# Kernel optimization log

Hardware: AMD Instinct MI355X
Metric: run time of the kernel (lower is better)

## Reference

```python
import jax, jax.numpy as jnp
import numpy as np

N = 20000
E = 500000
NS = 128
NT = 128
BN_EPS = 1e-3
DIMS = [NS, 2 * NT, 4 * NT, 2 * NT, NT, NT]


def setup_inputs() -> dict:
    key = jax.random.key(0)
    ks = jax.random.split(key, 32)
    inp = {
        "x": jax.random.normal(ks[0], (N, NS), jnp.float32),
        "edge_index": jax.random.randint(ks[1], (2, E), 0, N),
        "edge_attr": jax.random.uniform(ks[2], (E,), jnp.float32),
    }
    for i in range(5):
        din, dout = DIMS[i], DIMS[i + 1]
        inp[f"W{i+1}"] = jax.random.normal(ks[3 + i], (din, dout), jnp.float32) * (1.0 / np.sqrt(din)).astype(np.float32)
        inp[f"b{i+1}"] = jnp.zeros((dout,), jnp.float32)
    for i in range(4):
        d = DIMS[i + 1]
        inp[f"g{i+1}"] = 1.0 + 0.1 * jax.random.normal(ks[10 + i], (d,), jnp.float32)
        inp[f"be{i+1}"] = 0.1 * jax.random.normal(ks[14 + i], (d,), jnp.float32)
        inp[f"m{i+1}"] = 0.1 * jax.random.normal(ks[18 + i], (d,), jnp.float32)
        inp[f"v{i+1}"] = jax.random.uniform(ks[22 + i], (d,), jnp.float32, minval=0.5, maxval=1.5)
    return inp


def gcn_norm(edge_index, edge_attr, n):
    # PyG gcn_norm with self-loops (fill value 1) and symmetric degree norm.
    loop = jnp.arange(n)
    row = jnp.concatenate([edge_index[0], loop])
    col = jnp.concatenate([edge_index[1], loop])
    w = jnp.concatenate([edge_attr, jnp.ones((n,), edge_attr.dtype)])
    deg = jax.ops.segment_sum(w, col, num_segments=n)
    dinv = jnp.where(deg > 0, jax.lax.rsqrt(deg), 0.0)
    return row, col, dinv[row] * w * dinv[col]


def gcn_conv(h, W, b, row, col, norm, n):
    # out[col] += norm * (h @ W)[row]; then add bias (PyG GCNConv).
    hw = h @ W
    agg = jax.ops.segment_sum(hw[row] * norm[:, None], col, num_segments=n)
    return agg + b


def bn_eval(h, g, be, m, v):
    return (h - m) * jax.lax.rsqrt(v + BN_EPS) * g + be


def reference(x, edge_index, edge_attr,
              W1, b1, W2, b2, W3, b3, W4, b4, W5, b5,
              g1, be1, m1, v1, g2, be2, m2, v2,
              g3, be3, m3, v3, g4, be4, m4, v4):
    n = x.shape[0]
    row, col, norm = gcn_norm(edge_index, edge_attr, n)  # cached=True: shared by all layers
    h = jax.nn.sigmoid(bn_eval(gcn_conv(x, W1, b1, row, col, norm, n), g1, be1, m1, v1))
    h = jax.nn.sigmoid(bn_eval(gcn_conv(h, W2, b2, row, col, norm, n), g2, be2, m2, v2))
    h = jax.nn.sigmoid(bn_eval(gcn_conv(h, W3, b3, row, col, norm, n), g3, be3, m3, v3))
    h = jax.nn.sigmoid(bn_eval(gcn_conv(h, W4, b4, row, col, norm, n), g4, be4, m4, v4))
    h = jax.nn.sigmoid(gcn_conv(h, W5, b5, row, col, norm, n))
    # dropout is identity in eval mode
    x11 = h.T @ h  # [NT, NT]
    x12 = 0.5 * (x11 + x11.T)
    return x12 - jnp.diag(jnp.diag(x12))
```

## Files before the change

### kernel.cpp

```cpp
#include <hip/hip_runtime.h>
#include <hip/hip_bf16.h>
#include <hip/hip_fp8.h>
#include <cstdint>
#include <cstddef>

typedef __hip_bfloat16 bf16;
typedef unsigned char fp8;
typedef __attribute__((ext_vector_type(8))) short short8;
typedef __attribute__((ext_vector_type(4))) float f32x4;
typedef __attribute__((ext_vector_type(2))) float f32x2;

#define NSF 128
#define BN_EPS 1e-3f
#define NR 4
#define SCK 2048


__global__ void passA_kernel(const int* __restrict__ ei, int* __restrict__ fill,
                             int* __restrict__ loc, int E, int n, int rsize) {
    int idx = blockIdx.x * blockDim.x + threadIdx.x;
    if (idx < E) {
        int r = ei[idx];
        int c = ei[E + idx];
        int slot = c * NR + r / rsize;
        loc[idx] = atomicAdd(&fill[slot], 1);
    } else if (idx < E + n) {
        int i = idx - E;
        int slot = i * NR + i / rsize;
        loc[idx] = atomicAdd(&fill[slot], 1);
    }
}


__global__ void scan1_kernel(const int* __restrict__ cnt, int* __restrict__ blksum, int total) {
    __shared__ int red[256];
    int base = blockIdx.x * SCK + threadIdx.x * 8;
    int s = 0;
    #pragma unroll
    for (int i = 0; i < 8; ++i) {
        int idx = base + i;
        if (idx < total) s += cnt[idx];
    }
    red[threadIdx.x] = s;
    __syncthreads();
    for (int off2 = 128; off2 > 0; off2 >>= 1) {
        if (threadIdx.x < off2) red[threadIdx.x] += red[threadIdx.x + off2];
        __syncthreads();
    }
    if (threadIdx.x == 0) blksum[blockIdx.x] = red[0];
}

__global__ void scan2_kernel(int* __restrict__ blksum, int* __restrict__ row_ptr,
                             int nblk, int total) {
    __shared__ int part[256];
    int tid = threadIdx.x;
    int v = (tid < nblk) ? blksum[tid] : 0;
    part[tid] = v;
    __syncthreads();
    for (int off2 = 1; off2 < 256; off2 <<= 1) {
        int t = (tid >= off2) ? part[tid - off2] : 0;
        __syncthreads();
        part[tid] += t;
        __syncthreads();
    }
    if (tid < nblk) blksum[tid] = part[tid] - v;
    if (tid == 255) row_ptr[total] = part[255];
}

__global__ void scan3_kernel(const int* __restrict__ cnt, const int* __restrict__ blkoff,
                             int* __restrict__ row_ptr, int total) {
    __shared__ int part[256];
    int tid = threadIdx.x;
    int base = blockIdx.x * SCK + tid * 8;
    int loc[8]; int s = 0;
    #pragma unroll
    for (int i = 0; i < 8; ++i) {
        int idx = base + i;
        loc[i] = (idx < total) ? cnt[idx] : 0;
        s += loc[i];
    }
    part[tid] = s;
    __syncthreads();
    for (int off2 = 1; off2 < 256; off2 <<= 1) {
        int t = (tid >= off2) ? part[tid - off2] : 0;
        __syncthreads();
        part[tid] += t;
        __syncthreads();
    }
    int run = blkoff[blockIdx.x] + part[tid] - s;
    #pragma unroll
    for (int i = 0; i < 8; ++i) {
        int idx = base + i;
        if (idx < total) { row_ptr[idx] = run; run += loc[i]; }
    }
}

__global__ void passB_kernel(const int* __restrict__ ei, const float* __restrict__ ea,
                             const int* __restrict__ row_ptr, const int* __restrict__ loc,
                             int2* __restrict__ e8, int* __restrict__ csr_col,
                             int E, int n, int rsize) {
    int idx = blockIdx.x * blockDim.x + threadIdx.x;
    if (idx < E) {
        int r = ei[idx];
        int c = ei[E + idx];
        int slot = c * NR + r / rsize;
        int p = row_ptr[slot] + loc[idx];
        int2 rec; rec.x = r; rec.y = __float_as_int(ea[idx]);
        e8[p] = rec;
        csr_col[p] = c;
    } else if (idx < E + n) {
        int i = idx - E;
        int slot = i * NR + i / rsize;
        int p = row_ptr[slot] + loc[idx];
        int2 rec; rec.x = i; rec.y = __float_as_int(1.0f);
        e8[p] = rec;
        csr_col[p] = i;
    }
}

__global__ void degdinv_kernel(const int* __restrict__ row_ptr, const int2* __restrict__ e8,
                               float* __restrict__ dinv, int n) {
    int node = blockIdx.x * blockDim.x + threadIdx.x;
    if (node < n) {
        int s = row_ptr[node * NR], e = row_ptr[(node + 1) * NR];
        float d = 0.0f;
        for (int j = s; j < e; ++j) d += __int_as_float(e8[j].y);
        dinv[node] = (d > 0.0f) ? rsqrtf(d) : 0.0f;
    }
}

__global__ void normw_kernel(const float* __restrict__ dinv, const int* __restrict__ csr_col,
                             int2* __restrict__ e8, int EN) {
    int p = blockIdx.x * blockDim.x + threadIdx.x;
    if (p < EN) {
        int2 rec = e8[p];
        float w = dinv[rec.x] * __int_as_float(rec.y) * dinv[csr_col[p]];
        ((int*)e8)[2 * p + 1] = __float_as_int(w);
    }
}


__device__ inline void store_val(bf16* C, size_t idx, float a) {
    C[idx] = __float2bfloat16(a);
}
__device__ inline void store_val(fp8* C, size_t idx, float a) {
    int packed = __builtin_amdgcn_cvt_pk_fp8_f32(a, a, 0, false);
    C[idx] = (fp8)(packed & 0xff);
}

__global__ void prep_kernel(int* __restrict__ fill, int total,
                            const float* __restrict__ x, fp8* __restrict__ xq, int xcnt,
                            const float* __restrict__ W0, const float* __restrict__ W1,
                            const float* __restrict__ W2, const float* __restrict__ W3,
                            const float* __restrict__ W4,
                            bf16* __restrict__ wtbuf, int wtelems) {
    int idx = blockIdx.x * blockDim.x + threadIdx.x;
    if (idx < total) { fill[idx] = 0; return; }
    idx -= total;
    if (idx < xcnt) {
        store_val(xq, idx, x[idx]);
        return;
    }
    int widx = idx - xcnt;
    if (widx >= wtelems) return;
    const float* W; int K, off;
    if (widx < 32768)       { W = W0; K = 128; off = 0; }
    else if (widx < 163840) { W = W1; K = 256; off = 32768; }
    else if (widx < 294912) { W = W2; K = 512; off = 163840; }
    else if (widx < 327680) { W = W3; K = 256; off = 294912; }
    else                    { W = W4; K = 128; off = 327680; }
    int N2;
    if (widx < 32768) N2 = 256; else if (widx < 163840) N2 = 512;
    else if (widx < 294912) N2 = 256; else N2 = 128;
    int l = widx - off;
    int nn = l / K, kk = l % K;
    wtbuf[widx] = __float2bfloat16(W[(size_t)kk * N2 + nn]);
}


__device__ inline void gl_lds16(const bf16* g, bf16* l) {
    __builtin_amdgcn_global_load_lds(
        (const __attribute__((address_space(1))) void*)g,
        (__attribute__((address_space(3))) void*)l,
        16, 0, 0);
}


template <typename OT>
__global__ __launch_bounds__(256) void mfma_gemm_kernel(
    const bf16* __restrict__ A, const bf16* __restrict__ Wt,
    OT* __restrict__ C, int M, int K, int N, int mode,
    const float* __restrict__ bias, const float* __restrict__ g,
    const float* __restrict__ be, const float* __restrict__ m,
    const float* __restrict__ v) {
    __shared__ bf16 As[64][32];
    __shared__ bf16 Bs[128][32];
    int m0 = blockIdx.x * 64;
    int n0 = blockIdx.y * 128;
    int tid = threadIdx.x;
    int wave = tid >> 6, lane = tid & 63;
    int lrow = lane & 15, quad = lane >> 4;

    f32x4 acc[4][2] = {};

    int srow = lane >> 2;
    int sseg = lane & 3;
    int am = wave * 16 + srow;
    int bn = wave * 32 + srow;
    bool aok = (m0 + am) < M;

    for (int k0 = 0; k0 < K; k0 += 32) {
        if (aok)
            gl_lds16(A + (size_t)(m0 + am) * K + k0 + sseg * 8, &As[am][sseg * 8]);
        gl_lds16(Wt + (size_t)(n0 + bn) * K + k0 + sseg * 8, &Bs[bn][sseg * 8]);
        gl_lds16(Wt + (size_t)(n0 + bn + 16) * K + k0 + sseg * 8, &Bs[bn + 16][sseg * 8]);
        __syncthreads();

        short8 afrag[4], bfrag[2];
        #pragma unroll
        for (int mt = 0; mt < 4; ++mt)
            afrag[mt] = *(const short8*)(&As[mt * 16 + lrow][quad * 8]);
        #pragma unroll
        for (int nt = 0; nt < 2; ++nt)
            bfrag[nt] = *(const short8*)(&Bs[wave * 32 + nt * 16 + lrow][quad * 8]);
        #pragma unroll
        for (int mt = 0; mt < 4; ++mt)
            #pragma unroll
            for (int nt = 0; nt < 2; ++nt)
                acc[mt][nt] = __builtin_amdgcn_mfma_f32_16x16x32_bf16(
                    afrag[mt], bfrag[nt], acc[mt][nt], 0, 0, 0);
        __syncthreads();
    }
    #pragma unroll
    for (int nt = 0; nt < 2; ++nt) {
        int gn = n0 + wave * 32 + nt * 16 + lrow;
        float bsc = 0.0f, scale = 1.0f, mean = 0.0f, beta = 0.0f;
        if (mode == 1) {
            bsc = bias[gn];
            scale = g[gn] * rsqrtf(v[gn] + BN_EPS);
            mean = m[gn];
            beta = be[gn];
        }
        #pragma unroll
        for (int mt = 0; mt < 4; ++mt) {
            #pragma unroll
            for (int rr = 0; rr < 4; ++rr) {
                int gm = m0 + mt * 16 + quad * 4 + rr;
                if (gm < M) {
                    float a = acc[mt][nt][rr];
                    if (mode == 1) {
                        a = (a + bsc - mean) * scale + beta;
                        a = 1.0f / (1.0f + __expf(-a));
                    }
                    store_val(C, (size_t)gm * N + gn, a);
                }
            }
        }
    }
}


template <int VEC> struct F8Vec;
template <> struct F8Vec<2> { typedef unsigned short T; };
template <> struct F8Vec<4> { typedef unsigned int T; };

__device__ inline void fma_f8(unsigned short q, float w, float* acc) {
    f32x2 lo = __builtin_amdgcn_cvt_pk_f32_fp8((unsigned int)q, false);
    acc[0] += w * lo.x;
    acc[1] += w * lo.y;
}
__device__ inline void fma_f8(unsigned int q, float w, float* acc) {
    f32x2 lo = __builtin_amdgcn_cvt_pk_f32_fp8(q, false);
    f32x2 hi = __builtin_amdgcn_cvt_pk_f32_fp8(q, true);
    acc[0] += w * lo.x;
    acc[1] += w * lo.y;
    acc[2] += w * hi.x;
    acc[3] += w * hi.y;
}

template <int VEC>
__global__ __launch_bounds__(256) void agg_fp8_kernel(
    const fp8* __restrict__ hw,
    const int* __restrict__ row_ptr, const int2* __restrict__ e8,
    const float* __restrict__ bias,
    const float* __restrict__ g, const float* __restrict__ be,
    const float* __restrict__ m, const float* __restrict__ v,
    bf16* __restrict__ out, int n, int mode) {
    typedef typename F8Vec<VEC>::T T;
    const int dfeat = VEC * 64;
    __shared__ int2 recs[4][64];
    int wave = threadIdx.x >> 6;
    int lane = threadIdx.x & 63;
    int node = blockIdx.x * 4 + wave;
    if (node >= n) return;
    int s = row_ptr[node * NR], e = row_ptr[(node + 1) * NR];
    float acc[VEC];
    #pragma unroll
    for (int i = 0; i < VEC; ++i) acc[i] = 0.0f;
    const unsigned int base = (unsigned int)lane * VEC;

#define LOADG(Q, WV, J0)                                                     \
    _Pragma("unroll")                                                        \
    for (int u = 0; u < 8; ++u) {                                            \
        int2 rec = recs[wave][(J0) + u];                                     \
        WV[u] = __int_as_float(rec.y);                                       \
        Q[u] = *(const T*)(hw + ((unsigned int)rec.x * dfeat + base));       \
    }
#define CONSUME(Q, WV)                                                       \
    _Pragma("unroll")                                                        \
    for (int u = 0; u < 8; ++u) fma_f8(Q[u], WV[u], acc);

    for (int cs = s; cs < e; cs += 64) {
        int cnt = e - cs; if (cnt > 64) cnt = 64;
        int2 r0; r0.x = 0; r0.y = 0;
        if (lane < cnt) r0 = e8[cs + lane];
        recs[wave][lane] = r0;
        asm volatile("s_waitcnt vmcnt(0) lgkmcnt(0)" ::: "memory");

        int npad = (cnt + 15) & ~15;
        T qA[8], qB[8];
        float wA[8], wB[8];
        LOADG(qA, wA, 0)
        LOADG(qB, wB, 8)
        for (int j0 = 16; j0 < npad; j0 += 16) {
            CONSUME(qA, wA)
            LOADG(qA, wA, j0)
            CONSUME(qB, wB)
            LOADG(qB, wB, j0 + 8)
        }
        CONSUME(qA, wA)
        CONSUME(qB, wB)
    }
#undef LOADG
#undef CONSUME

    #pragma unroll
    for (int i = 0; i < VEC; ++i) {
        int f = (int)base + i;
        float a = acc[i];
        if (mode != 0) {
            a += bias[f];
            if (mode == 1) {
                float scale = g[f] * rsqrtf(v[f] + BN_EPS);
                a = (a - m[f]) * scale + be[f];
            }
            a = 1.0f / (1.0f + __expf(-a));
        }
        out[(size_t)node * dfeat + f] = __float2bfloat16(a);
    }
}

#define TPAD 8

__global__ __launch_bounds__(256) void htht_mfma_kernel(
    const bf16* __restrict__ h, float* __restrict__ partial, int n) {
    __shared__ bf16 hsT[128][32 + TPAD];
    int b = blockIdx.x;
    int tid = threadIdx.x;
    int wave = tid >> 6, lane = tid & 63;
    int lrow = lane & 15, quad = lane >> 4;

    f32x4 acc[2][8] = {};

    int kk = tid >> 3;
    int seg = tid & 7;

    for (int kt = 0; kt < 8; ++kt) {
        int k0 = b * 256 + kt * 32;
        #pragma unroll
        for (int s2 = 0; s2 < 2; ++s2) {
            int fs = (seg + s2 * 8) * 8;
            int gk = k0 + kk;
            uint4 q; q.x = q.y = q.z = q.w = 0u;
            if (gk < n) q = *(const uint4*)(h + (size_t)gk * 128 + fs);
            const unsigned short* u = (const unsigned short*)&q;
            #pragma unroll
            for (int i = 0; i < 8; ++i)
                *((unsigned short*)&hsT[fs + i][kk]) = u[i];
        }
        __syncthreads();
        short8 af0 = *(const short8*)(&hsT[wave * 32 + lrow][quad * 8]);
        short8 af1 = *(const short8*)(&hsT[wave * 32 + 16 + lrow][quad * 8]);
        #pragma unroll
        for (int t = 0; t < 8; ++t) {
            short8 bfrag = *(const short8*)(&hsT[t * 16 + lrow][quad * 8]);
            acc[0][t] = __builtin_amdgcn_mfma_f32_16x16x32_bf16(af0, bfrag, acc[0][t], 0, 0, 0);
            acc[1][t] = __builtin_amdgcn_mfma_f32_16x16x32_bf16(af1, bfrag, acc[1][t], 0, 0, 0);
        }
        __syncthreads();
    }
    float* p = partial + (size_t)b * 16384;
    #pragma unroll
    for (int a_ = 0; a_ < 2; ++a_) {
        #pragma unroll
        for (int t = 0; t < 8; ++t) {
            #pragma unroll
            for (int rr = 0; rr < 4; ++rr) {
                int gm = wave * 32 + a_ * 16 + quad * 4 + rr;
                int gn = t * 16 + lrow;
                p[gm * 128 + gn] = acc[a_][t][rr];
            }
        }
    }
}

__global__ void reduce_kernel(const float* __restrict__ partial, float* __restrict__ out, int nchunks) {
    int idx = blockIdx.x * blockDim.x + threadIdx.x;
    float s = 0.0f;
    for (int c = 0; c < nchunks; ++c) s += partial[(size_t)c * 16384 + idx];
    int i = idx / 128, j = idx % 128;
    out[idx] = (i == j) ? 0.0f : s;
}

extern "C" void kernel_launch(void* const* d_in, const int* in_sizes, int n_in,
                              void* d_out, int out_size, void* d_ws, size_t ws_size,
                              hipStream_t stream) {
    const float* x  = (const float*)d_in[0];
    const int*   ei = (const int*)d_in[1];
    const float* ea = (const float*)d_in[2];
    const float* W[5];  const float* bvec[5];
    for (int l = 0; l < 5; ++l) { W[l] = (const float*)d_in[3 + 2 * l]; bvec[l] = (const float*)d_in[4 + 2 * l]; }
    const float* g[4]; const float* be[4]; const float* mm[4]; const float* vv[4];
    for (int l = 0; l < 4; ++l) {
        g[l]  = (const float*)d_in[13 + 4 * l];
        be[l] = (const float*)d_in[14 + 4 * l];
        mm[l] = (const float*)d_in[15 + 4 * l];
        vv[l] = (const float*)d_in[16 + 4 * l];
    }
    const int n = in_sizes[0] / NSF;
    const int E = in_sizes[1] / 2;
    const int EN = E + n;
    const int rsize = (n + NR - 1) / NR;
    const int total = n * NR;
    const int nscan = (total + SCK - 1) / SCK;
    const int dims[6] = {128, 256, 512, 256, 128, 128};
    const int wtoff[5] = {0, 32768, 163840, 294912, 327680};
    const int wtelems = 344064;

    auto align = [](size_t o) { return (o + 255) & ~(size_t)255; };
    size_t off = 0;
    float* dinv    = (float*)((char*)d_ws + off); off = align(off + (size_t)n * 4);
    int*   fill    = (int*)  ((char*)d_ws + off); off = align(off + (size_t)total * 4);
    int*   row_ptr = (int*)  ((char*)d_ws + off); off = align(off + ((size_t)total + 1) * 4);
    int*   blksum  = (int*)  ((char*)d_ws + off); off = align(off + (size_t)256 * 4);
    int*   locb    = (int*)  ((char*)d_ws + off); off = align(off + (size_t)EN * 4);
    int2*  e8      = (int2*) ((char*)d_ws + off); off = align(off + (size_t)EN * 8);
    int*   csr_col = (int*)  ((char*)d_ws + off); off = align(off + (size_t)EN * 4);
    bf16*  wtbuf   = (bf16*) ((char*)d_ws + off); off = align(off + (size_t)wtelems * 2);
    fp8*   xq      = (fp8*)  ((char*)d_ws + off); off = align(off + (size_t)n * 128);
    bf16*  hbuf    = (bf16*) ((char*)d_ws + off); off = align(off + (size_t)n * 512 * 2);
    bf16*  abuf    = (bf16*) ((char*)d_ws + off); off = align(off + (size_t)n * 512 * 2);
    fp8*   f8buf   = (fp8*)  ((char*)d_ws + off); off = align(off + (size_t)n * 256);
    const int KCH = (20000 + 255) / 256;
    float* partial = (float*)((char*)d_ws + off); off = align(off + (size_t)KCH * 16384 * 4);

    {
        int xcnt = n * 128;
        int items = total + xcnt + wtelems;
        prep_kernel<<<(items + 255) / 256, 256, 0, stream>>>(fill, total, x, xq, xcnt,
            W[0], W[1], W[2], W[3], W[4], wtbuf, wtelems);
    }

    passA_kernel<<<(EN + 255) / 256, 256, 0, stream>>>(ei, fill, locb, E, n, rsize);
    scan1_kernel<<<nscan, 256, 0, stream>>>(fill, blksum, total);
    scan2_kernel<<<1, 256, 0, stream>>>(blksum, row_ptr, nscan, total);
    scan3_kernel<<<nscan, 256, 0, stream>>>(fill, blksum, row_ptr, total);
    passB_kernel<<<(EN + 255) / 256, 256, 0, stream>>>(ei, ea, row_ptr, locb,
                                                       e8, csr_col, E, n, rsize);
    degdinv_kernel<<<(n + 255) / 256, 256, 0, stream>>>(row_ptr, e8, dinv, n);
    normw_kernel<<<(EN + 255) / 256, 256, 0, stream>>>(dinv, csr_col, e8, EN);

    int ablocks = (n + 3) / 4;
    auto gemm_bf16 = [&](const bf16* A, int l, bf16* C, int mode) {
        int K = dims[l], N = dims[l + 1];
        dim3 gg((n + 63) / 64, N / 128);
        int bi = (l < 4) ? l : 0;
        mfma_gemm_kernel<bf16><<<gg, 256, 0, stream>>>(A, wtbuf + wtoff[l], C, n, K, N, mode,
                                                       bvec[l], g[bi], be[bi], mm[bi], vv[bi]);
    };
    auto gemm_fp8 = [&](const bf16* A, int l, fp8* C, int mode) {
        int K = dims[l], N = dims[l + 1];
        dim3 gg((n + 63) / 64, N / 128);
        int bi = (l < 4) ? l : 0;
        mfma_gemm_kernel<fp8><<<gg, 256, 0, stream>>>(A, wtbuf + wtoff[l], C, n, K, N, mode,
                                                      bvec[l], g[bi], be[bi], mm[bi], vv[bi]);
    };

    agg_fp8_kernel<2><<<ablocks, 256, 0, stream>>>(xq, row_ptr, e8,
        bvec[0], bvec[0], bvec[0], bvec[0], bvec[0], abuf, n, 0);
    gemm_fp8(abuf, 0, f8buf, 1);
    agg_fp8_kernel<4><<<ablocks, 256, 0, stream>>>(f8buf, row_ptr, e8,
        bvec[1], bvec[1], bvec[1], bvec[1], bvec[1], abuf, n, 0);
    gemm_bf16(abuf, 1, hbuf, 1);
    gemm_fp8(hbuf, 2, f8buf, 0);
    agg_fp8_kernel<4><<<ablocks, 256, 0, stream>>>(f8buf, row_ptr, e8,
        bvec[2], g[2], be[2], mm[2], vv[2], abuf, n, 1);
    gemm_fp8(abuf, 3, f8buf, 0);
    agg_fp8_kernel<2><<<ablocks, 256, 0, stream>>>(f8buf, row_ptr, e8,
        bvec[3], g[3], be[3], mm[3], vv[3], hbuf, n, 1);
    gemm_fp8(hbuf, 4, f8buf, 0);
    agg_fp8_kernel<2><<<ablocks, 256, 0, stream>>>(f8buf, row_ptr, e8,
        bvec[4], bvec[4], bvec[4], bvec[4], bvec[4], abuf, n, 2);

    htht_mfma_kernel<<<KCH, 256, 0, stream>>>(abuf, partial, n);
    reduce_kernel<<<16384 / 256, 256, 0, stream>>>(partial, (float*)d_out, KCH);
}
```

Before: 380.9 us.

## Use 16-byte fp8 gathers per lane with multi-edge wave split and shuffle reduction

The fp8 aggregation kernel is restructured so each lane loads 16 fp8 features (uint4) instead of 2 or 4 bytes. A wave now processes several edges at once (8 edges for the 128-wide layer, 4 for the 256-wide), with lane groups covering one row each, and finishes with a cross-group shuffle reduction. Only group-0 lanes run the epilogue, writing 16 bf16 values with vector stores. The aim is fewer, wider memory transactions for the gathers, at the cost of a larger accumulator (16 floats per lane), extra shuffle-reduction work, and wasted lanes when a node's edge count does not fill the groups.

New measurement: 454.3 us. +19.3%, slower.

```diff
diff --git a/kernel.cpp b/kernel.cpp
--- a/kernel.cpp
+++ b/kernel.cpp
@@ -260,22 +260,21 @@
 }
 
 
-template <int VEC> struct F8Vec;
-template <> struct F8Vec<2> { typedef unsigned short T; };
-template <> struct F8Vec<4> { typedef unsigned int T; };
-
-__device__ inline void fma_f8(unsigned short q, float w, float* acc) {
-    f32x2 lo = __builtin_amdgcn_cvt_pk_f32_fp8((unsigned int)q, false);
-    acc[0] += w * lo.x;
-    acc[1] += w * lo.y;
-}
-__device__ inline void fma_f8(unsigned int q, float w, float* acc) {
-    f32x2 lo = __builtin_amdgcn_cvt_pk_f32_fp8(q, false);
-    f32x2 hi = __builtin_amdgcn_cvt_pk_f32_fp8(q, true);
-    acc[0] += w * lo.x;
-    acc[1] += w * lo.y;
-    acc[2] += w * hi.x;
-    acc[3] += w * hi.y;
+template <int VEC> struct AggCfg;
+template <> struct AggCfg<2> { static const int EPI = 8; static const int LPE = 8;  };
+template <> struct AggCfg<4> { static const int EPI = 4; static const int LPE = 16; };
+
+__device__ inline void fma16_f8(uint4 q, float w, float* acc) {
+    const unsigned* qq = reinterpret_cast<const unsigned*>(&q);
+    #pragma unroll
+    for (int c = 0; c < 4; ++c) {
+        f32x2 lo = __builtin_amdgcn_cvt_pk_f32_fp8(qq[c], false);
+        f32x2 hi = __builtin_amdgcn_cvt_pk_f32_fp8(qq[c], true);
+        acc[c * 4 + 0] += w * lo.x;
+        acc[c * 4 + 1] += w * lo.y;
+        acc[c * 4 + 2] += w * hi.x;
+        acc[c * 4 + 3] += w * hi.y;
+    }
 }
 
 template <int VEC>
@@ -286,29 +285,31 @@
     const float* __restrict__ g, const float* __restrict__ be,
     const float* __restrict__ m, const float* __restrict__ v,
     bf16* __restrict__ out, int n, int mode) {
-    typedef typename F8Vec<VEC>::T T;
     const int dfeat = VEC * 64;
+    const int EPI = AggCfg<VEC>::EPI;
+    const int LPE = AggCfg<VEC>::LPE;
     __shared__ int2 recs[4][64];
     int wave = threadIdx.x >> 6;
     int lane = threadIdx.x & 63;
     int node = blockIdx.x * 4 + wave;
     if (node >= n) return;
     int s = row_ptr[node * NR], e = row_ptr[(node + 1) * NR];
-    float acc[VEC];
-    #pragma unroll
-    for (int i = 0; i < VEC; ++i) acc[i] = 0.0f;
-    const unsigned int base = (unsigned int)lane * VEC;
-
-#define LOADG(Q, WV, J0)                                                     \
-    _Pragma("unroll")                                                        \
-    for (int u = 0; u < 8; ++u) {                                            \
-        int2 rec = recs[wave][(J0) + u];                                     \
-        WV[u] = __int_as_float(rec.y);                                       \
-        Q[u] = *(const T*)(hw + ((unsigned int)rec.x * dfeat + base));       \
-    }
-#define CONSUME(Q, WV)                                                       \
-    _Pragma("unroll")                                                        \
-    for (int u = 0; u < 8; ++u) fma_f8(Q[u], WV[u], acc);
+    int grp = lane / LPE;
+    int sub = lane % LPE;
+
+    float acc[16];
+    #pragma unroll
+    for (int k = 0; k < 16; ++k) acc[k] = 0.0f;
+
+    const fp8* hw_base = hw + sub * 16;
+
+#define LOADI(Q, WV, T)                                                       \
+    {                                                                         \
+        int2 rc = recs[wave][(T) * EPI + grp];                                \
+        WV = __int_as_float(rc.y);                                            \
+        Q = *(const uint4*)(hw_base + ((size_t)(unsigned)rc.x * dfeat));      \
+    }
+#define CONSI(Q, WV) fma16_f8(Q, WV, acc);
 
     for (int cs = s; cs < e; cs += 64) {
         int cnt = e - cs; if (cnt > 64) cnt = 64;
@@ -317,36 +318,58 @@
         recs[wave][lane] = r0;
         asm volatile("s_waitcnt vmcnt(0) lgkmcnt(0)" ::: "memory");
 
-        int npad = (cnt + 15) & ~15;
-        T qA[8], qB[8];
-        float wA[8], wB[8];
-        LOADG(qA, wA, 0)
-        LOADG(qB, wB, 8)
-        for (int j0 = 16; j0 < npad; j0 += 16) {
-            CONSUME(qA, wA)
-            LOADG(qA, wA, j0)
-            CONSUME(qB, wB)
-            LOADG(qB, wB, j0 + 8)
-        }
-        CONSUME(qA, wA)
-        CONSUME(qB, wB)
-    }
-#undef LOADG
-#undef CONSUME
-
-    #pragma unroll
-    for (int i = 0; i < VEC; ++i) {
-        int f = (int)base + i;
-        float a = acc[i];
-        if (mode != 0) {
-            a += bias[f];
-            if (mode == 1) {
-                float scale = g[f] * rsqrtf(v[f] + BN_EPS);
-                a = (a - m[f]) * scale + be[f];
+        int ni = (cnt + EPI - 1) / EPI;
+        int ni4 = (ni + 3) & ~3;
+
+        uint4 qA, qB, qC, qD;
+        float wA, wB, wC, wD;
+        LOADI(qA, wA, 0)
+        LOADI(qB, wB, 1)
+        LOADI(qC, wC, 2)
+        LOADI(qD, wD, 3)
+        for (int t = 4; t < ni4; t += 4) {
+            CONSI(qA, wA) LOADI(qA, wA, t)
+            CONSI(qB, wB) LOADI(qB, wB, t + 1)
+            CONSI(qC, wC) LOADI(qC, wC, t + 2)
+            CONSI(qD, wD) LOADI(qD, wD, t + 3)
+        }
+        CONSI(qA, wA)
+        CONSI(qB, wB)
+        CONSI(qC, wC)
+        CONSI(qD, wD)
+    }
+#undef LOADI
+#undef CONSI
+
+    #pragma unroll
+    for (int k = 0; k < 16; ++k) {
+        float vsum = acc[k];
+        if (EPI == 8) vsum += __shfl_xor(vsum, 8);
+        vsum += __shfl_xor(vsum, 16);
+        vsum += __shfl_xor(vsum, 32);
+        acc[k] = vsum;
+    }
+
+    if (grp == 0) {
+        int f0 = sub * 16;
+        bf16 ob[16];
+        #pragma unroll
+        for (int k = 0; k < 16; ++k) {
+            int f = f0 + k;
+            float a = acc[k];
+            if (mode != 0) {
+                a += bias[f];
+                if (mode == 1) {
+                    float scale = g[f] * rsqrtf(v[f] + BN_EPS);
+                    a = (a - m[f]) * scale + be[f];
+                }
+                a = 1.0f / (1.0f + __expf(-a));
             }
-            a = 1.0f / (1.0f + __expf(-a));
-        }
-        out[(size_t)node * dfeat + f] = __float2bfloat16(a);
+            ob[k] = __float2bfloat16(a);
+        }
+        bf16* op = out + (size_t)node * dfeat + f0;
+        *(uint4*)(op) = *(const uint4*)(&ob[0]);
+        *(uint4*)(op + 8) = *(const uint4*)(&ob[8]);
     }
 }
 
```
